# Performance work log

Measured on AMD Instinct MI355X. Metric: run time of the kernel, lower is better.

The kernel has to match this reference:

```python
import math
import jax, jax.numpy as jnp
import numpy as np

SDE_THRESHOLD = 10.0
ANGLE_THRESHOLD_DEG = 30.0


def setup_inputs() -> dict:
    key = jax.random.key(0)
    k1, k2 = jax.random.split(key)
    B, H, N = 8, 16, 1024
    y_pred = jax.random.normal(k1, (B, H, 4), dtype=jnp.float32)
    sample_points = jax.random.normal(k2, (B, N, 3), dtype=jnp.float32)
    return {"y_pred": y_pred, "sample_points": sample_points}


def reference(y_pred, sample_points):
    # y_pred: [B,H,4] = (nx,ny,nz,d) per plane head; sample_points: [B,N,3]
    B, H, _ = y_pred.shape
    n = y_pred[..., :3]
    n = n / jnp.linalg.norm(n, axis=-1, keepdims=True)  # normalize normals
    d = y_pred[..., 3]

    # transform_representation_cm: represent plane by (normal, point) where
    # point = projection of the point-cloud centroid onto the plane n.x + d = 0
    cm = sample_points.mean(axis=1)  # [B,3]
    point = cm[:, None, :] - (jnp.einsum('bhd,bd->bh', n, cm) + d)[..., None] * n  # [B,H,3]

    # chamfer_adapter: reflect points across each plane, bidirectional chamfer (squared dists)
    proj = jnp.einsum('bnd,bhd->bhn', sample_points, n) + d[:, :, None]  # [B,H,N]
    refl = sample_points[:, None, :, :] - 2.0 * proj[..., None] * n[:, :, None, :]  # [B,H,N,3]
    rr = jnp.sum(refl * refl, axis=-1)                  # [B,H,N]
    ss = jnp.sum(sample_points * sample_points, axis=-1)  # [B,N]
    cross = jnp.einsum('bhid,bjd->bhij', refl, sample_points)  # [B,H,N,N]
    d2 = rr[..., None] + ss[:, None, None, :] - 2.0 * cross
    sde = jnp.min(d2, axis=-1).mean(axis=-1) + jnp.min(d2, axis=-2).mean(axis=-1)  # [B,H]

    # minmax_normalization -> confidence = 1 - (sde - min) / |max - min| per batch row
    mn = sde.min(axis=1, keepdims=True)
    mx = sde.max(axis=1, keepdims=True)
    conf = 1.0 - (sde - mn) / jnp.abs(mx - mn)

    # pairwise angle-based duplicate suppression (vectorized NMS)
    cos = jnp.clip(jnp.einsum('bhd,bgd->bhg', n, n), -1.0, 1.0)
    ang = jnp.arccos(cos) * (180.0 / math.pi)
    close = (ang < ANGLE_THRESHOLD_DEG) | (180.0 - ang < ANGLE_THRESHOLD_DEG)
    close = close & ~jnp.eye(H, dtype=bool)
    valid = sde <= SDE_THRESHOLD  # filter x.sde <= sde_threshold
    # plane i is popped iff exists valid j (close) with sde_i >= sde_j (equal sde pops both)
    sup = valid & jnp.any(close & valid[:, None, :] & (sde[:, :, None] >= sde[:, None, :]), axis=-1)
    keep = valid & ~sup

    # to_tensor(): [normal(3), point(3), confidence, sde]; sort kept by confidence desc,
    # zero-pad suppressed/filtered slots (fixed shape [B,H,8] instead of ragged pad_sequence)
    planes = jnp.concatenate([n, point, conf[..., None], sde[..., None]], axis=-1)  # [B,H,8]
    sort_key = jnp.where(keep, conf, -jnp.inf)
    order = jnp.argsort(-sort_key, axis=1)
    planes_s = jnp.take_along_axis(planes, order[..., None], axis=1)
    keep_s = jnp.take_along_axis(keep, order, axis=1)
    return jnp.where(keep_s[..., None], planes_s, 0.0)
```

## Files before the change

kernel.cpp:

```cpp
#include <hip/hip_runtime.h>
#include <math.h>

#define BB 8
#define HH 16
#define NN 1024
#define TB 256
#define POWN 2
#define OCH 512
#define SCH 512


__global__ __launch_bounds__(TB) void chamfer_kernel(
    const float* __restrict__ y_pred,
    const float* __restrict__ sp,
    float* __restrict__ ws)
{
    __shared__ __align__(16) float4 pts[SCH];

    const int blk = blockIdx.x;
    const int bh  = blk >> 2;
    const int oh  = (blk >> 1) & 1;
    const int sh  = blk & 1;
    const int b   = bh >> 4;
    const int tid = threadIdx.x;

    float pnx = y_pred[bh * 4 + 0];
    float pny = y_pred[bh * 4 + 1];
    float pnz = y_pred[bh * 4 + 2];
    float pd  = y_pred[bh * 4 + 3];
    float inv = 1.0f / sqrtf(pnx * pnx + pny * pny + pnz * pnz);
    pnx *= inv; pny *= inv; pnz *= inv;

    const float* spb = sp + (size_t)b * NN * 3;

    for (int k = tid; k < SCH; k += TB) {
        int j = sh * SCH + k;
        float x = spb[j * 3 + 0], y = spb[j * 3 + 1], z = spb[j * 3 + 2];
        pts[k] = make_float4(x, y, z, x * x + y * y + z * z);
    }

    float mx[POWN], my[POWN], mz[POWN], osq[POWN];
#pragma unroll
    for (int u = 0; u < POWN; ++u) {
        int i = oh * OCH + u * TB + tid;
        float x = spb[i * 3 + 0], y = spb[i * 3 + 1], z = spb[i * 3 + 2];
        float proj = x * pnx + y * pny + z * pnz + pd;
        x -= 2.0f * proj * pnx;
        y -= 2.0f * proj * pny;
        z -= 2.0f * proj * pnz;
        osq[u] = x * x + y * y + z * z;
        mx[u] = -2.0f * x; my[u] = -2.0f * y; mz[u] = -2.0f * z;
    }
    __syncthreads();

    float m0[POWN], m1[POWN], m2[POWN], m3[POWN];
#pragma unroll
    for (int u = 0; u < POWN; ++u) { m0[u] = 3.4e38f; m1[u] = 3.4e38f; m2[u] = 3.4e38f; m3[u] = 3.4e38f; }

    for (int j = 0; j < SCH; j += 4) {
        float4 qa = pts[j + 0];
        float4 qb = pts[j + 1];
        float4 qc = pts[j + 2];
        float4 qd = pts[j + 3];
#pragma unroll
        for (int u = 0; u < POWN; ++u) {
            m0[u] = fminf(m0[u], fmaf(mx[u], qa.x, fmaf(my[u], qa.y, fmaf(mz[u], qa.z, qa.w))));
            m1[u] = fminf(m1[u], fmaf(mx[u], qb.x, fmaf(my[u], qb.y, fmaf(mz[u], qb.z, qb.w))));
            m2[u] = fminf(m2[u], fmaf(mx[u], qc.x, fmaf(my[u], qc.y, fmaf(mz[u], qc.z, qc.w))));
            m3[u] = fminf(m3[u], fmaf(mx[u], qd.x, fmaf(my[u], qd.y, fmaf(mz[u], qd.z, qd.w))));
        }
    }

    float* wp = ws + ((size_t)(bh * 2 + sh)) * NN + oh * OCH;
#pragma unroll
    for (int u = 0; u < POWN; ++u)
        wp[u * TB + tid] = osq[u] + fminf(fminf(m0[u], m1[u]), fminf(m2[u], m3[u]));
}

__global__ __launch_bounds__(TB) void finalize_kernel(
    const float* __restrict__ ws,
    const float* __restrict__ y_pred,
    const float* __restrict__ sp,
    float* __restrict__ out)
{
    const int b   = blockIdx.x;
    const int tid = threadIdx.x;

    __shared__ float sde_s[HH], nx_s[HH], ny_s[HH], nz_s[HH], d_s[HH], conf_s[HH];
    __shared__ float cmacc[3];
    __shared__ int keep_s[HH];

    if (tid < HH) sde_s[tid] = 0.0f;
    if (tid < 3)  cmacc[tid] = 0.0f;
    __syncthreads();

    const float* spb = sp + (size_t)b * NN * 3;
    float sx = 0.0f, sy = 0.0f, sz = 0.0f;
    for (int p = tid; p < NN; p += TB) {
        sx += spb[p * 3 + 0];
        sy += spb[p * 3 + 1];
        sz += spb[p * 3 + 2];
    }
    for (int off = 32; off; off >>= 1) {
        sx += __shfl_down(sx, off, 64);
        sy += __shfl_down(sy, off, 64);
        sz += __shfl_down(sz, off, 64);
    }
    if ((tid & 63) == 0) {
        atomicAdd(&cmacc[0], sx);
        atomicAdd(&cmacc[1], sy);
        atomicAdd(&cmacc[2], sz);
    }

    {
        const int h   = tid >> 4;
        const int sub = tid & 15;
        const float* p0 = ws + ((size_t)((b * HH + h) * 2 + 0)) * NN;
        const float* p1 = ws + ((size_t)((b * HH + h) * 2 + 1)) * NN;
        float acc = 0.0f;
        for (int k = 0; k < 64; ++k) {
            int i = sub * 64 + k;
            acc += fminf(p0[i], p1[i]);
        }
        atomicAdd(&sde_s[h], acc);
    }
    __syncthreads();

    const float cmx = cmacc[0] / NN, cmy = cmacc[1] / NN, cmz = cmacc[2] / NN;

    if (tid < HH) {
        int h = tid;
        float nx = y_pred[(b * HH + h) * 4 + 0];
        float ny = y_pred[(b * HH + h) * 4 + 1];
        float nz = y_pred[(b * HH + h) * 4 + 2];
        float d  = y_pred[(b * HH + h) * 4 + 3];
        float inv = 1.0f / sqrtf(nx * nx + ny * ny + nz * nz);
        nx *= inv; ny *= inv; nz *= inv;
        nx_s[h] = nx; ny_s[h] = ny; nz_s[h] = nz; d_s[h] = d;
        sde_s[h] = sde_s[h] * (2.0f / NN);
    }
    __syncthreads();

    if (tid < HH) {
        int h = tid;
        float mn = sde_s[0], mx = sde_s[0];
        for (int g = 1; g < HH; ++g) {
            mn = fminf(mn, sde_s[g]);
            mx = fmaxf(mx, sde_s[g]);
        }
        float sde  = sde_s[h];
        float conf = 1.0f - (sde - mn) / fabsf(mx - mn);
        conf_s[h]  = conf;
        bool valid = (sde <= 10.0f);
        bool sup   = false;
        if (valid) {
            for (int g = 0; g < HH; ++g) {
                if (g == h) continue;
                float c = nx_s[h] * nx_s[g] + ny_s[h] * ny_s[g] + nz_s[h] * nz_s[g];
                c = fminf(1.0f, fmaxf(-1.0f, c));
                float ang = acosf(c) * 57.29577951308232f;
                bool close = (ang < 30.0f) || (180.0f - ang < 30.0f);
                if (close && (sde_s[g] <= 10.0f) && (sde >= sde_s[g])) sup = true;
            }
        }
        keep_s[h] = (valid && !sup) ? 1 : 0;
    }
    __syncthreads();

    if (tid < HH) {
        int h = tid;
        float keyh = keep_s[h] ? conf_s[h] : -INFINITY;
        int pos = 0;
        for (int g = 0; g < HH; ++g) {
            float keyg = keep_s[g] ? conf_s[g] : -INFINITY;
            if (keyg > keyh || (keyg == keyh && g < h)) ++pos;
        }
        float nx = nx_s[h], ny = ny_s[h], nz = nz_s[h];
        float t  = nx * cmx + ny * cmy + nz * cmz + d_s[h];
        float px = cmx - t * nx, py = cmy - t * ny, pz = cmz - t * nz;

        float* o = out + (size_t)(b * HH + pos) * 8;
        if (keep_s[h]) {
            o[0] = nx; o[1] = ny; o[2] = nz;
            o[3] = px; o[4] = py; o[5] = pz;
            o[6] = conf_s[h];
            o[7] = sde_s[h];
        } else {
            for (int c = 0; c < 8; ++c) o[c] = 0.0f;
        }
    }
}

extern "C" void kernel_launch(void* const* d_in, const int* in_sizes, int n_in,
                              void* d_out, int out_size, void* d_ws, size_t ws_size,
                              hipStream_t stream) {
    const float* y_pred = (const float*)d_in[0];
    const float* sp     = (const float*)d_in[1];
    float* out          = (float*)d_out;
    float* ws           = (float*)d_ws;

    chamfer_kernel<<<dim3(BB * HH * 4), dim3(TB), 0, stream>>>(y_pred, sp, ws);
    finalize_kernel<<<dim3(BB), dim3(TB), 0, stream>>>(ws, y_pred, sp, out);
}
```

Before: 78.41 us.

## Repartition chamfer blocks: each block owns all queries over a quarter of sources

```diff
diff --git a/kernel.cpp b/kernel.cpp
--- a/kernel.cpp
+++ b/kernel.cpp
@@ -5,9 +5,9 @@
 #define HH 16
 #define NN 1024
 #define TB 256
-#define POWN 2
-#define OCH 512
-#define SCH 512
+#define POWN 4
+#define SCH 256
+#define SHN 4
 
 
 __global__ __launch_bounds__(TB) void chamfer_kernel(
@@ -19,8 +19,7 @@
 
     const int blk = blockIdx.x;
     const int bh  = blk >> 2;
-    const int oh  = (blk >> 1) & 1;
-    const int sh  = blk & 1;
+    const int sh  = blk & 3;
     const int b   = bh >> 4;
     const int tid = threadIdx.x;
 
@@ -33,16 +32,16 @@
 
     const float* spb = sp + (size_t)b * NN * 3;
 
-    for (int k = tid; k < SCH; k += TB) {
-        int j = sh * SCH + k;
+    {
+        int j = sh * SCH + tid;
         float x = spb[j * 3 + 0], y = spb[j * 3 + 1], z = spb[j * 3 + 2];
-        pts[k] = make_float4(x, y, z, x * x + y * y + z * z);
+        pts[tid] = make_float4(x, y, z, x * x + y * y + z * z);
     }
 
     float mx[POWN], my[POWN], mz[POWN], osq[POWN];
 #pragma unroll
     for (int u = 0; u < POWN; ++u) {
-        int i = oh * OCH + u * TB + tid;
+        int i = u * TB + tid;
         float x = spb[i * 3 + 0], y = spb[i * 3 + 1], z = spb[i * 3 + 2];
         float proj = x * pnx + y * pny + z * pnz + pd;
         x -= 2.0f * proj * pnx;
@@ -71,7 +70,7 @@
         }
     }
 
-    float* wp = ws + ((size_t)(bh * 2 + sh)) * NN + oh * OCH;
+    float* wp = ws + ((size_t)(bh * SHN + sh)) * NN;
 #pragma unroll
     for (int u = 0; u < POWN; ++u)
         wp[u * TB + tid] = osq[u] + fminf(fminf(m0[u], m1[u]), fminf(m2[u], m3[u]));
@@ -112,17 +111,20 @@
         atomicAdd(&cmacc[2], sz);
     }
 
-    {
-        const int h   = tid >> 4;
-        const int sub = tid & 15;
-        const float* p0 = ws + ((size_t)((b * HH + h) * 2 + 0)) * NN;
-        const float* p1 = ws + ((size_t)((b * HH + h) * 2 + 1)) * NN;
-        float acc = 0.0f;
-        for (int k = 0; k < 64; ++k) {
-            int i = sub * 64 + k;
-            acc += fminf(p0[i], p1[i]);
-        }
-        atomicAdd(&sde_s[h], acc);
+    for (int h = 0; h < HH; ++h) {
+        const float4* p0 = (const float4*)(ws + ((size_t)((b * HH + h) * SHN + 0)) * NN);
+        const float4* p1 = (const float4*)(ws + ((size_t)((b * HH + h) * SHN + 1)) * NN);
+        const float4* p2 = (const float4*)(ws + ((size_t)((b * HH + h) * SHN + 2)) * NN);
+        const float4* p3 = (const float4*)(ws + ((size_t)((b * HH + h) * SHN + 3)) * NN);
+        float4 a = p0[tid], c = p1[tid], d = p2[tid], e = p3[tid];
+        float4 m;
+        m.x = fminf(fminf(a.x, c.x), fminf(d.x, e.x));
+        m.y = fminf(fminf(a.y, c.y), fminf(d.y, e.y));
+        m.z = fminf(fminf(a.z, c.z), fminf(d.z, e.z));
+        m.w = fminf(fminf(a.w, c.w), fminf(d.w, e.w));
+        float acc = (m.x + m.y) + (m.z + m.w);
+        for (int off = 32; off; off >>= 1) acc += __shfl_down(acc, off, 64);
+        if ((tid & 63) == 0) atomicAdd(&sde_s[h], acc);
     }
     __syncthreads();
 
@@ -199,6 +201,6 @@
     float* out          = (float*)d_out;
     float* ws           = (float*)d_ws;
 
-    chamfer_kernel<<<dim3(BB * HH * 4), dim3(TB), 0, stream>>>(y_pred, sp, ws);
+    chamfer_kernel<<<dim3(BB * HH * SHN), dim3(TB), 0, stream>>>(y_pred, sp, ws);
     finalize_kernel<<<dim3(BB), dim3(TB), 0, stream>>>(ws, y_pred, sp, out);
 }
```

Result: slower. 86.82 us (+10.7%).

## Fuse chamfer and finalize kernels with last-block atomic counter

Applied to the files above, without the earlier changes.

```diff
diff --git a/kernel.cpp b/kernel.cpp
--- a/kernel.cpp
+++ b/kernel.cpp
@@ -8,14 +8,19 @@
 #define POWN 2
 #define OCH 512
 #define SCH 512
-
-
-__global__ __launch_bounds__(TB) void chamfer_kernel(
+#define GRID (BB * HH * 4)
+
+#define WS_PART_FLOATS (BB * HH * 2 * NN)
+
+__global__ __launch_bounds__(TB) void fused_kernel(
     const float* __restrict__ y_pred,
     const float* __restrict__ sp,
-    float* __restrict__ ws)
+    float* __restrict__ ws,
+    unsigned int* __restrict__ counter,
+    float* __restrict__ out)
 {
     __shared__ __align__(16) float4 pts[SCH];
+    __shared__ int is_last_s;
 
     const int blk = blockIdx.x;
     const int bh  = blk >> 2;
@@ -24,67 +29,69 @@
     const int b   = bh >> 4;
     const int tid = threadIdx.x;
 
-    float pnx = y_pred[bh * 4 + 0];
-    float pny = y_pred[bh * 4 + 1];
-    float pnz = y_pred[bh * 4 + 2];
-    float pd  = y_pred[bh * 4 + 3];
-    float inv = 1.0f / sqrtf(pnx * pnx + pny * pny + pnz * pnz);
-    pnx *= inv; pny *= inv; pnz *= inv;
-
-    const float* spb = sp + (size_t)b * NN * 3;
-
-    for (int k = tid; k < SCH; k += TB) {
-        int j = sh * SCH + k;
-        float x = spb[j * 3 + 0], y = spb[j * 3 + 1], z = spb[j * 3 + 2];
-        pts[k] = make_float4(x, y, z, x * x + y * y + z * z);
+    {
+        float pnx = y_pred[bh * 4 + 0];
+        float pny = y_pred[bh * 4 + 1];
+        float pnz = y_pred[bh * 4 + 2];
+        float pd  = y_pred[bh * 4 + 3];
+        float inv = 1.0f / sqrtf(pnx * pnx + pny * pny + pnz * pnz);
+        pnx *= inv; pny *= inv; pnz *= inv;
+
+        const float* spb = sp + (size_t)b * NN * 3;
+
+        for (int k = tid; k < SCH; k += TB) {
+            int j = sh * SCH + k;
+            float x = spb[j * 3 + 0], y = spb[j * 3 + 1], z = spb[j * 3 + 2];
+            pts[k] = make_float4(x, y, z, x * x + y * y + z * z);
+        }
+
+        float mx[POWN], my[POWN], mz[POWN], osq[POWN];
+#pragma unroll
+        for (int u = 0; u < POWN; ++u) {
+            int i = oh * OCH + u * TB + tid;
+            float x = spb[i * 3 + 0], y = spb[i * 3 + 1], z = spb[i * 3 + 2];
+            float proj = x * pnx + y * pny + z * pnz + pd;
+            x -= 2.0f * proj * pnx;
+            y -= 2.0f * proj * pny;
+            z -= 2.0f * proj * pnz;
+            osq[u] = x * x + y * y + z * z;
+            mx[u] = -2.0f * x; my[u] = -2.0f * y; mz[u] = -2.0f * z;
+        }
+        __syncthreads();
+
+        float m0[POWN], m1[POWN], m2[POWN], m3[POWN];
+#pragma unroll
+        for (int u = 0; u < POWN; ++u) { m0[u] = 3.4e38f; m1[u] = 3.4e38f; m2[u] = 3.4e38f; m3[u] = 3.4e38f; }
+
+        for (int j = 0; j < SCH; j += 4) {
+            float4 qa = pts[j + 0];
+            float4 qb = pts[j + 1];
+            float4 qc = pts[j + 2];
+            float4 qd = pts[j + 3];
+#pragma unroll
+            for (int u = 0; u < POWN; ++u) {
+                m0[u] = fminf(m0[u], fmaf(mx[u], qa.x, fmaf(my[u], qa.y, fmaf(mz[u], qa.z, qa.w))));
+                m1[u] = fminf(m1[u], fmaf(mx[u], qb.x, fmaf(my[u], qb.y, fmaf(mz[u], qb.z, qb.w))));
+                m2[u] = fminf(m2[u], fmaf(mx[u], qc.x, fmaf(my[u], qc.y, fmaf(mz[u], qc.z, qc.w))));
+                m3[u] = fminf(m3[u], fmaf(mx[u], qd.x, fmaf(my[u], qd.y, fmaf(mz[u], qd.z, qd.w))));
+            }
+        }
+
+        float* wp = ws + ((size_t)(bh * 2 + sh)) * NN + oh * OCH;
+#pragma unroll
+        for (int u = 0; u < POWN; ++u)
+            wp[u * TB + tid] = osq[u] + fminf(fminf(m0[u], m1[u]), fminf(m2[u], m3[u]));
     }
 
-    float mx[POWN], my[POWN], mz[POWN], osq[POWN];
-#pragma unroll
-    for (int u = 0; u < POWN; ++u) {
-        int i = oh * OCH + u * TB + tid;
-        float x = spb[i * 3 + 0], y = spb[i * 3 + 1], z = spb[i * 3 + 2];
-        float proj = x * pnx + y * pny + z * pnz + pd;
-        x -= 2.0f * proj * pnx;
-        y -= 2.0f * proj * pny;
-        z -= 2.0f * proj * pnz;
-        osq[u] = x * x + y * y + z * z;
-        mx[u] = -2.0f * x; my[u] = -2.0f * y; mz[u] = -2.0f * z;
+    __syncthreads();
+    if (tid == 0) {
+        __threadfence();
+        unsigned int old = atomicAdd(counter, 1u);
+        is_last_s = (old == (unsigned int)(GRID - 1)) ? 1 : 0;
     }
     __syncthreads();
-
-    float m0[POWN], m1[POWN], m2[POWN], m3[POWN];
-#pragma unroll
-    for (int u = 0; u < POWN; ++u) { m0[u] = 3.4e38f; m1[u] = 3.4e38f; m2[u] = 3.4e38f; m3[u] = 3.4e38f; }
-
-    for (int j = 0; j < SCH; j += 4) {
-        float4 qa = pts[j + 0];
-        float4 qb = pts[j + 1];
-        float4 qc = pts[j + 2];
-        float4 qd = pts[j + 3];
-#pragma unroll
-        for (int u = 0; u < POWN; ++u) {
-            m0[u] = fminf(m0[u], fmaf(mx[u], qa.x, fmaf(my[u], qa.y, fmaf(mz[u], qa.z, qa.w))));
-            m1[u] = fminf(m1[u], fmaf(mx[u], qb.x, fmaf(my[u], qb.y, fmaf(mz[u], qb.z, qb.w))));
-            m2[u] = fminf(m2[u], fmaf(mx[u], qc.x, fmaf(my[u], qc.y, fmaf(mz[u], qc.z, qc.w))));
-            m3[u] = fminf(m3[u], fmaf(mx[u], qd.x, fmaf(my[u], qd.y, fmaf(mz[u], qd.z, qd.w))));
-        }
-    }
-
-    float* wp = ws + ((size_t)(bh * 2 + sh)) * NN + oh * OCH;
-#pragma unroll
-    for (int u = 0; u < POWN; ++u)
-        wp[u * TB + tid] = osq[u] + fminf(fminf(m0[u], m1[u]), fminf(m2[u], m3[u]));
-}
-
-__global__ __launch_bounds__(TB) void finalize_kernel(
-    const float* __restrict__ ws,
-    const float* __restrict__ y_pred,
-    const float* __restrict__ sp,
-    float* __restrict__ out)
-{
-    const int b   = blockIdx.x;
-    const int tid = threadIdx.x;
+    if (!is_last_s) return;
+    __threadfence();
 
     __shared__ float sde_s[HH], nx_s[HH], ny_s[HH], nz_s[HH], d_s[HH], conf_s[HH];
     __shared__ float cmacc[3];
@@ -94,100 +101,103 @@
     if (tid < 3)  cmacc[tid] = 0.0f;
     __syncthreads();
 
-    const float* spb = sp + (size_t)b * NN * 3;
-    float sx = 0.0f, sy = 0.0f, sz = 0.0f;
-    for (int p = tid; p < NN; p += TB) {
-        sx += spb[p * 3 + 0];
-        sy += spb[p * 3 + 1];
-        sz += spb[p * 3 + 2];
-    }
-    for (int off = 32; off; off >>= 1) {
-        sx += __shfl_down(sx, off, 64);
-        sy += __shfl_down(sy, off, 64);
-        sz += __shfl_down(sz, off, 64);
-    }
-    if ((tid & 63) == 0) {
-        atomicAdd(&cmacc[0], sx);
-        atomicAdd(&cmacc[1], sy);
-        atomicAdd(&cmacc[2], sz);
-    }
-
-    {
-        const int h   = tid >> 4;
-        const int sub = tid & 15;
-        const float* p0 = ws + ((size_t)((b * HH + h) * 2 + 0)) * NN;
-        const float* p1 = ws + ((size_t)((b * HH + h) * 2 + 1)) * NN;
-        float acc = 0.0f;
-        for (int k = 0; k < 64; ++k) {
-            int i = sub * 64 + k;
-            acc += fminf(p0[i], p1[i]);
-        }
-        atomicAdd(&sde_s[h], acc);
-    }
-    __syncthreads();
-
-    const float cmx = cmacc[0] / NN, cmy = cmacc[1] / NN, cmz = cmacc[2] / NN;
-
-    if (tid < HH) {
-        int h = tid;
-        float nx = y_pred[(b * HH + h) * 4 + 0];
-        float ny = y_pred[(b * HH + h) * 4 + 1];
-        float nz = y_pred[(b * HH + h) * 4 + 2];
-        float d  = y_pred[(b * HH + h) * 4 + 3];
-        float inv = 1.0f / sqrtf(nx * nx + ny * ny + nz * nz);
-        nx *= inv; ny *= inv; nz *= inv;
-        nx_s[h] = nx; ny_s[h] = ny; nz_s[h] = nz; d_s[h] = d;
-        sde_s[h] = sde_s[h] * (2.0f / NN);
-    }
-    __syncthreads();
-
-    if (tid < HH) {
-        int h = tid;
-        float mn = sde_s[0], mx = sde_s[0];
-        for (int g = 1; g < HH; ++g) {
-            mn = fminf(mn, sde_s[g]);
-            mx = fmaxf(mx, sde_s[g]);
-        }
-        float sde  = sde_s[h];
-        float conf = 1.0f - (sde - mn) / fabsf(mx - mn);
-        conf_s[h]  = conf;
-        bool valid = (sde <= 10.0f);
-        bool sup   = false;
-        if (valid) {
+    for (int bb = 0; bb < BB; ++bb) {
+        const float* spb = sp + (size_t)bb * NN * 3;
+        float sx = 0.0f, sy = 0.0f, sz = 0.0f;
+        for (int p = tid; p < NN; p += TB) {
+            sx += spb[p * 3 + 0];
+            sy += spb[p * 3 + 1];
+            sz += spb[p * 3 + 2];
+        }
+        for (int off = 32; off; off >>= 1) {
+            sx += __shfl_down(sx, off, 64);
+            sy += __shfl_down(sy, off, 64);
+            sz += __shfl_down(sz, off, 64);
+        }
+        if ((tid & 63) == 0) {
+            atomicAdd(&cmacc[0], sx);
+            atomicAdd(&cmacc[1], sy);
+            atomicAdd(&cmacc[2], sz);
+        }
+
+        for (int h = 0; h < HH; ++h) {
+            const float4* p0 = (const float4*)(ws + ((size_t)((bb * HH + h) * 2 + 0)) * NN);
+            const float4* p1 = (const float4*)(ws + ((size_t)((bb * HH + h) * 2 + 1)) * NN);
+            float4 a = p0[tid], c = p1[tid];
+            float acc = (fminf(a.x, c.x) + fminf(a.y, c.y)) +
+                        (fminf(a.z, c.z) + fminf(a.w, c.w));
+            for (int off = 32; off; off >>= 1) acc += __shfl_down(acc, off, 64);
+            if ((tid & 63) == 0) atomicAdd(&sde_s[h], acc);
+        }
+        __syncthreads();
+
+        const float cmx = cmacc[0] / NN, cmy = cmacc[1] / NN, cmz = cmacc[2] / NN;
+
+        if (tid < HH) {
+            int h = tid;
+            float nx = y_pred[(bb * HH + h) * 4 + 0];
+            float ny = y_pred[(bb * HH + h) * 4 + 1];
+            float nz = y_pred[(bb * HH + h) * 4 + 2];
+            float d  = y_pred[(bb * HH + h) * 4 + 3];
+            float inv = 1.0f / sqrtf(nx * nx + ny * ny + nz * nz);
+            nx *= inv; ny *= inv; nz *= inv;
+            nx_s[h] = nx; ny_s[h] = ny; nz_s[h] = nz; d_s[h] = d;
+            sde_s[h] = sde_s[h] * (2.0f / NN);
+        }
+        __syncthreads();
+
+        if (tid < HH) {
+            int h = tid;
+            float mn = sde_s[0], mx = sde_s[0];
+            for (int g = 1; g < HH; ++g) {
+                mn = fminf(mn, sde_s[g]);
+                mx = fmaxf(mx, sde_s[g]);
+            }
+            float sde  = sde_s[h];
+            float conf = 1.0f - (sde - mn) / fabsf(mx - mn);
+            conf_s[h]  = conf;
+            bool valid = (sde <= 10.0f);
+            bool sup   = false;
+            if (valid) {
+                for (int g = 0; g < HH; ++g) {
+                    if (g == h) continue;
+                    float c = nx_s[h] * nx_s[g] + ny_s[h] * ny_s[g] + nz_s[h] * nz_s[g];
+                    c = fminf(1.0f, fmaxf(-1.0f, c));
+                    float ang = acosf(c) * 57.29577951308232f;
+                    bool close = (ang < 30.0f) || (180.0f - ang < 30.0f);
+                    if (close && (sde_s[g] <= 10.0f) && (sde >= sde_s[g])) sup = true;
+                }
+            }
+            keep_s[h] = (valid && !sup) ? 1 : 0;
+        }
+        __syncthreads();
+
+        if (tid < HH) {
+            int h = tid;
+            float keyh = keep_s[h] ? conf_s[h] : -INFINITY;
+            int pos = 0;
             for (int g = 0; g < HH; ++g) {
-                if (g == h) continue;
-                float c = nx_s[h] * nx_s[g] + ny_s[h] * ny_s[g] + nz_s[h] * nz_s[g];
-                c = fminf(1.0f, fmaxf(-1.0f, c));
-                float ang = acosf(c) * 57.29577951308232f;
-                bool close = (ang < 30.0f) || (180.0f - ang < 30.0f);
-                if (close && (sde_s[g] <= 10.0f) && (sde >= sde_s[g])) sup = true;
-            }
-        }
-        keep_s[h] = (valid && !sup) ? 1 : 0;
-    }
-    __syncthreads();
-
-    if (tid < HH) {
-        int h = tid;
-        float keyh = keep_s[h] ? conf_s[h] : -INFINITY;
-        int pos = 0;
-        for (int g = 0; g < HH; ++g) {
-            float keyg = keep_s[g] ? conf_s[g] : -INFINITY;
-            if (keyg > keyh || (keyg == keyh && g < h)) ++pos;
-        }
-        float nx = nx_s[h], ny = ny_s[h], nz = nz_s[h];
-        float t  = nx * cmx + ny * cmy + nz * cmz + d_s[h];
-        float px = cmx - t * nx, py = cmy - t * ny, pz = cmz - t * nz;
-
-        float* o = out + (size_t)(b * HH + pos) * 8;
-        if (keep_s[h]) {
-            o[0] = nx; o[1] = ny; o[2] = nz;
-            o[3] = px; o[4] = py; o[5] = pz;
-            o[6] = conf_s[h];
-            o[7] = sde_s[h];
-        } else {
-            for (int c = 0; c < 8; ++c) o[c] = 0.0f;
-        }
+                float keyg = keep_s[g] ? conf_s[g] : -INFINITY;
+                if (keyg > keyh || (keyg == keyh && g < h)) ++pos;
+            }
+            float nx = nx_s[h], ny = ny_s[h], nz = nz_s[h];
+            float t  = nx * cmx + ny * cmy + nz * cmz + d_s[h];
+            float px = cmx - t * nx, py = cmy - t * ny, pz = cmz - t * nz;
+
+            float* o = out + (size_t)(bb * HH + pos) * 8;
+            if (keep_s[h]) {
+                o[0] = nx; o[1] = ny; o[2] = nz;
+                o[3] = px; o[4] = py; o[5] = pz;
+                o[6] = conf_s[h];
+                o[7] = sde_s[h];
+            } else {
+                for (int c = 0; c < 8; ++c) o[c] = 0.0f;
+            }
+        }
+        __syncthreads();
+        if (tid < HH) sde_s[tid] = 0.0f;
+        if (tid < 3)  cmacc[tid] = 0.0f;
+        __syncthreads();
     }
 }
 
@@ -198,7 +208,8 @@
     const float* sp     = (const float*)d_in[1];
     float* out          = (float*)d_out;
     float* ws           = (float*)d_ws;
-
-    chamfer_kernel<<<dim3(BB * HH * 4), dim3(TB), 0, stream>>>(y_pred, sp, ws);
-    finalize_kernel<<<dim3(BB), dim3(TB), 0, stream>>>(ws, y_pred, sp, out);
+    unsigned int* cnt   = (unsigned int*)((char*)d_ws + (size_t)WS_PART_FLOATS * sizeof(float));
+
+    hipMemsetAsync(cnt, 0, sizeof(unsigned int), stream);
+    fused_kernel<<<dim3(GRID), dim3(TB), 0, stream>>>(y_pred, sp, ws, cnt, out);
 }
```

New measurement: 183.3 us. 2.34x slower.
